# Kernel optimization log

Measured on AMD Instinct MI355X. Metric: run time of the kernel, lower is better.

## Reference

```python
import jax, jax.numpy as jnp
import numpy as np

B, N, F, E, C, FC = 16, 5000, 512, 160000, 64, 128


def gcn_conv(x, src, dst, W, b, n_total):
    loop = jnp.arange(n_total, dtype=src.dtype)
    s = jnp.concatenate([src, loop])
    d = jnp.concatenate([dst, loop])
    deg = jax.ops.segment_sum(jnp.ones_like(s, dtype=x.dtype), d, num_segments=n_total)
    dinv = jnp.where(deg > 0, jax.lax.rsqrt(deg), 0.0)
    norm = dinv[s] * dinv[d]                      # [E']
    h = x @ W                                      # [n_total, out]
    msg = h[s] * norm[:, None]
    out = jax.ops.segment_sum(msg, d, num_segments=n_total)
    return out + b


def setup_inputs() -> dict:
    key = jax.random.key(0)
    ks = jax.random.split(key, 12)
    inp = {
        "node_features": jax.random.normal(ks[0], (B, N, F), jnp.float32),
        "col_features": jax.random.normal(ks[1], (B, C, FC), jnp.float32),
        "edge_index": jax.random.randint(ks[2], (2, E), 0, N, dtype=jnp.int64),
        # GCNConv 1/2 weights + node head
        "W1": jax.random.normal(ks[3], (F, 16), jnp.float32) / np.sqrt(F),
        "b1": jnp.zeros((16,), jnp.float32),
        "W2": jax.random.normal(ks[4], (16, 16), jnp.float32) / 4.0,
        "b2": jnp.zeros((16,), jnp.float32),
        "fc_w": jax.random.normal(ks[5], (16, 1), jnp.float32) / 4.0,
        "fc_b": jnp.zeros((1,), jnp.float32),
        # column MLP: Linear(FC,16) -> ReLU -> Linear(16,1)
        "cw1": jax.random.normal(ks[6], (FC, 16), jnp.float32) / np.sqrt(FC),
        "cb1": jnp.zeros((16,), jnp.float32),
        "cw2": jax.random.normal(ks[7], (16, 1), jnp.float32) / 4.0,
        "cb2": jnp.zeros((1,), jnp.float32),
    }
    return inp


def reference(node_features, col_features, edge_index, W1, b1, W2, b2, fc_w, fc_b, cw1, cb1, cw2, cb2):
    b, n, _ = node_features.shape
    n_total = b * n
    # batched edge_index via node-offset trick (shared graph per batch element)
    offsets = (jnp.arange(b, dtype=edge_index.dtype) * n)[:, None]   # [B,1]
    src = (edge_index[0][None, :] + offsets).reshape(-1)              # [B*E]
    dst = (edge_index[1][None, :] + offsets).reshape(-1)

    x = node_features.reshape(n_total, -1)
    x = jax.nn.relu(gcn_conv(x, src, dst, W1, b1, n_total))
    x = jax.nn.relu(gcn_conv(x, src, dst, W2, b2, n_total))
    node_logits = (x.reshape(b, n, 16) @ fc_w + fc_b)[..., 0]         # [B,N]

    h = jax.nn.relu(col_features @ cw1 + cb1)
    col_logits = (h @ cw2 + cb2)[..., 0]                              # [B,C]

    joint = node_logits[:, :, None] + col_logits[:, None, :]          # [B,N,C]
    return joint.reshape(b, -1)                                       # [B, N*C]
```

## Files before the change

### kernel.cpp

```cpp
#include <hip/hip_runtime.h>
#include <hip/hip_bf16.h>

typedef unsigned short u16;
typedef unsigned int   u32;

#define B_  16
#define N_  5000
#define F_  512
#define C_  64
#define FC_ 128
#define NT  (B_ * N_)

__device__ __forceinline__ float bf2f(u16 h) {
    return __uint_as_float(((u32)h) << 16);
}
__device__ __forceinline__ u16 f2bf(float f) {
    union { __hip_bfloat16 h; u16 s; } c; c.h = __float2bfloat16(f); return c.s;
}
__device__ __forceinline__ float ldw(const void* p, int i, int fF) {
    return fF ? bf2f(((const u16*)p)[i]) : ((const float*)p)[i];
}

__global__ __launch_bounds__(256) void det_k(const u32* __restrict__ x32,
                                             const u32* __restrict__ ei32,
                                             int* __restrict__ flags)
{
    __shared__ int cnt;
    if (threadIdx.x == 0) cnt = 0;
    __syncthreads();
    u32 w = x32[threadIdx.x];
    int e = (int)((w >> 7) & 0xffu);
    if (e >= 112 && e <= 136) atomicAdd(&cnt, 1);
    __syncthreads();
    if (threadIdx.x == 0) {
        flags[0] = (cnt >= 128) ? 1 : 0;
        u32 orv = 0;
        for (int i = 1; i < 64; i += 2) orv |= ei32[i];
        flags[1] = (orv == 0u) ? 1 : 0;
    }
}

__device__ __forceinline__ int src_at(const u32* ei32, int t, int E, int fI) {
    return (int)(fI ? ei32[2 * t] : ei32[t]);
}
__device__ __forceinline__ int dst_at(const u32* ei32, int t, int E, int fI) {
    return (int)(fI ? ei32[2 * (E + t)] : ei32[E + t]);
}

__global__ __launch_bounds__(256) void prep_weights(
    const void* __restrict__ W1, const void* __restrict__ W2,
    const void* __restrict__ fcw, const void* __restrict__ cw1,
    const void* __restrict__ cw2, const void* __restrict__ b1,
    const void* __restrict__ b2, const void* __restrict__ fcb,
    const void* __restrict__ cb1, const void* __restrict__ cb2,
    const int* __restrict__ flags,
    float* __restrict__ w1f, float* __restrict__ w2f, float* __restrict__ fcwf,
    float* __restrict__ cw1f, float* __restrict__ cw2f, float* __restrict__ b1f,
    float* __restrict__ b2f, float* __restrict__ fcbf, float* __restrict__ cb1f,
    float* __restrict__ cb2f)
{
    int fF = flags[0];
    int t = blockIdx.x * blockDim.x + threadIdx.x;
    if (t < 8192) { w1f[t] = ldw(W1, t, fF); return; }
    int u = t - 8192;
    if (u < 256)  { w2f[u]  = ldw(W2, u, fF);  return; }  u -= 256;
    if (u < 16)   { fcwf[u] = ldw(fcw, u, fF); return; }  u -= 16;
    if (u < 2048) { cw1f[u] = ldw(cw1, u, fF); return; }  u -= 2048;
    if (u < 16)   { cw2f[u] = ldw(cw2, u, fF); return; }  u -= 16;
    if (u < 16)   { b1f[u]  = ldw(b1, u, fF);  return; }  u -= 16;
    if (u < 16)   { b2f[u]  = ldw(b2, u, fF);  return; }  u -= 16;
    if (u < 1)    { fcbf[u] = ldw(fcb, u, fF); return; }  u -= 1;
    if (u < 16)   { cb1f[u] = ldw(cb1, u, fF); return; }  u -= 16;
    if (u < 1)    { cb2f[u] = ldw(cb2, u, fF); return; }
}

__global__ __launch_bounds__(256) void deg_k(const u32* __restrict__ ei32,
                                             const int* __restrict__ flags,
                                             int* __restrict__ deg, int E)
{
    int t = blockIdx.x * blockDim.x + threadIdx.x;
    if (t >= E) return;
    int d = dst_at(ei32, t, E, flags[1]);
    if ((unsigned)d < (unsigned)N_) atomicAdd(&deg[d], 1);
}

__global__ __launch_bounds__(1024) void scan_k(const int* __restrict__ deg,
                                               int* __restrict__ rowptr,
                                               int* __restrict__ cursor,
                                               float* __restrict__ dinv)
{
    __shared__ int ssum[1024];
    int t = threadIdx.x;
    int base = t * 5;
    int loc[5];
    int run = 0;
#pragma unroll
    for (int i = 0; i < 5; i++) {
        int idx = base + i;
        int v = (idx < N_) ? deg[idx] : 0;
        loc[i] = run;
        run += v;
    }
    ssum[t] = run;
    __syncthreads();
    for (int offs = 1; offs < 1024; offs <<= 1) {
        int v = (t >= offs) ? ssum[t - offs] : 0;
        __syncthreads();
        ssum[t] += v;
        __syncthreads();
    }
    int exclusive = ssum[t] - run;
#pragma unroll
    for (int i = 0; i < 5; i++) {
        int idx = base + i;
        if (idx < N_) {
            int rp = exclusive + loc[i];
            rowptr[idx] = rp;
            cursor[idx] = rp;
            dinv[idx] = 1.0f / sqrtf((float)deg[idx] + 1.0f);
        }
    }
    if (t == 1023) rowptr[N_] = ssum[1023];
}

__global__ __launch_bounds__(256) void fill_k(const u32* __restrict__ ei32,
                                              const int* __restrict__ flags,
                                              int* __restrict__ cursor,
                                              int* __restrict__ csr, int E)
{
    int t = blockIdx.x * blockDim.x + threadIdx.x;
    if (t >= E) return;
    int fI = flags[1];
    int s = src_at(ei32, t, E, fI);
    int d = dst_at(ei32, t, E, fI);
    if ((unsigned)d >= (unsigned)N_) return;
    if ((unsigned)s >= (unsigned)N_) s = 0;
    int pos = atomicAdd(&cursor[d], 1);
    if ((unsigned)pos < (unsigned)E) csr[pos] = s;
}

__global__ __launch_bounds__(256) void gemm1_k(const void* __restrict__ xraw,
                                               const float* __restrict__ w1f,
                                               const float* __restrict__ dinv,
                                               const int* __restrict__ flags,
                                               u16* __restrict__ out)
{
    int row = blockIdx.x * blockDim.x + threadIdx.x;
    if (row >= NT) return;
    float acc[16];
#pragma unroll
    for (int k = 0; k < 16; k++) acc[k] = 0.0f;

    if (flags[0]) {
        const u16* xr = (const u16*)xraw + (size_t)row * F_;
        for (int f = 0; f < F_; f += 8) {
            uint4 pk = *(const uint4*)(xr + f);
            u32 q[4] = {pk.x, pk.y, pk.z, pk.w};
#pragma unroll
            for (int j = 0; j < 4; j++) {
                float v0 = bf2f((u16)(q[j] & 0xffffu));
                float v1 = bf2f((u16)(q[j] >> 16));
                const float* w0 = w1f + (f + 2 * j) * 16;
#pragma unroll
                for (int k = 0; k < 16; k++) acc[k] += v0 * w0[k];
#pragma unroll
                for (int k = 0; k < 16; k++) acc[k] += v1 * w0[16 + k];
            }
        }
    } else {
        const float* xr = (const float*)xraw + (size_t)row * F_;
        for (int f = 0; f < F_; f += 8) {
            float4 a = *(const float4*)(xr + f);
            float4 b = *(const float4*)(xr + f + 4);
            float v[8] = {a.x, a.y, a.z, a.w, b.x, b.y, b.z, b.w};
#pragma unroll
            for (int j = 0; j < 8; j++) {
                const float* w0 = w1f + (f + j) * 16;
#pragma unroll
                for (int k = 0; k < 16; k++) acc[k] += v[j] * w0[k];
            }
        }
    }
    float s = dinv[row % N_];
    union { uint4 u; u16 h[8]; } o0, o1;
#pragma unroll
    for (int k = 0; k < 8; k++) o0.h[k] = f2bf(acc[k] * s);
#pragma unroll
    for (int k = 0; k < 8; k++) o1.h[k] = f2bf(acc[8 + k] * s);
    uint4* op = (uint4*)(out + (size_t)row * 16);
    op[0] = o0.u;
    op[1] = o1.u;
}

__global__ __launch_bounds__(256) void agg1_k(const u16* __restrict__ h,
                                              const int* __restrict__ rowptr,
                                              const int* __restrict__ csr,
                                              const float* __restrict__ dinv,
                                              const float* __restrict__ b1f,
                                              u16* __restrict__ out)
{
    int t = blockIdx.x * blockDim.x + threadIdx.x;
    int g = t >> 4;
    if (g >= NT) return;
    int k = t & 15;
    int d = g % N_;
    int b = g / N_;
    const u16* hb = h + (size_t)b * N_ * 16;
    float acc = bf2f(hb[d * 16 + k]);
    int e0 = rowptr[d], e1 = rowptr[d + 1];
    for (int e = e0; e < e1; e++) {
        int s = csr[e];
        acc += bf2f(hb[s * 16 + k]);
    }
    float v = acc * dinv[d] + b1f[k];
    out[(size_t)g * 16 + k] = f2bf(fmaxf(v, 0.0f));
}

__global__ __launch_bounds__(256) void gemm2_k(const u16* __restrict__ x1,
                                               const float* __restrict__ w2f,
                                               const float* __restrict__ dinv,
                                               u16* __restrict__ out)
{
    int row = blockIdx.x * blockDim.x + threadIdx.x;
    if (row >= NT) return;
    const uint4* xp = (const uint4*)(x1 + (size_t)row * 16);
    union { uint4 u; u16 h[8]; } i0, i1;
    i0.u = xp[0]; i1.u = xp[1];
    float xv[16];
#pragma unroll
    for (int j = 0; j < 8; j++) { xv[j] = bf2f(i0.h[j]); xv[8 + j] = bf2f(i1.h[j]); }
    float acc[16];
#pragma unroll
    for (int k = 0; k < 16; k++) acc[k] = 0.0f;
#pragma unroll
    for (int j = 0; j < 16; j++) {
        const float* wr = w2f + j * 16;
#pragma unroll
        for (int k = 0; k < 16; k++) acc[k] += xv[j] * wr[k];
    }
    float s = dinv[row % N_];
    union { uint4 u; u16 h[8]; } o0, o1;
#pragma unroll
    for (int k = 0; k < 8; k++) o0.h[k] = f2bf(acc[k] * s);
#pragma unroll
    for (int k = 0; k < 8; k++) o1.h[k] = f2bf(acc[8 + k] * s);
    uint4* op = (uint4*)(out + (size_t)row * 16);
    op[0] = o0.u;
    op[1] = o1.u;
}

__global__ __launch_bounds__(256) void agg2_k(const u16* __restrict__ h,
                                              const int* __restrict__ rowptr,
                                              const int* __restrict__ csr,
                                              const float* __restrict__ dinv,
                                              const float* __restrict__ b2f,
                                              const float* __restrict__ fcwf,
                                              const float* __restrict__ fcbf,
                                              float* __restrict__ nl)
{
    int t = blockIdx.x * blockDim.x + threadIdx.x;
    int g = t >> 4;
    if (g >= NT) return;
    int k = t & 15;
    int d = g % N_;
    int b = g / N_;
    const u16* hb = h + (size_t)b * N_ * 16;
    float acc = bf2f(hb[d * 16 + k]);
    int e0 = rowptr[d], e1 = rowptr[d + 1];
    for (int e = e0; e < e1; e++) {
        int s = csr[e];
        acc += bf2f(hb[s * 16 + k]);
    }
    float v = fmaxf(acc * dinv[d] + b2f[k], 0.0f);
    float p = v * fcwf[k];
    p += __shfl_xor(p, 8, 16);
    p += __shfl_xor(p, 4, 16);
    p += __shfl_xor(p, 2, 16);
    p += __shfl_xor(p, 1, 16);
    if (k == 0) nl[g] = p + fcbf[0];
}

__global__ __launch_bounds__(256) void col_k(const void* __restrict__ cfraw,
                                             const float* __restrict__ cw1f,
                                             const float* __restrict__ cb1f,
                                             const float* __restrict__ cw2f,
                                             const float* __restrict__ cb2f,
                                             const int* __restrict__ flags,
                                             float* __restrict__ cl)
{
    int t = blockIdx.x * blockDim.x + threadIdx.x;
    if (t >= B_ * C_) return;
    float acc[16];
#pragma unroll
    for (int k = 0; k < 16; k++) acc[k] = cb1f[k];
    if (flags[0]) {
        const u16* r = (const u16*)cfraw + (size_t)t * FC_;
        for (int f = 0; f < FC_; f += 8) {
            uint4 pk = *(const uint4*)(r + f);
            u32 q[4] = {pk.x, pk.y, pk.z, pk.w};
#pragma unroll
            for (int j = 0; j < 4; j++) {
                float v0 = bf2f((u16)(q[j] & 0xffffu));
                float v1 = bf2f((u16)(q[j] >> 16));
                const float* w0 = cw1f + (f + 2 * j) * 16;
#pragma unroll
                for (int k = 0; k < 16; k++) acc[k] += v0 * w0[k];
#pragma unroll
                for (int k = 0; k < 16; k++) acc[k] += v1 * w0[16 + k];
            }
        }
    } else {
        const float* r = (const float*)cfraw + (size_t)t * FC_;
        for (int f = 0; f < FC_; f += 4) {
            float4 a = *(const float4*)(r + f);
            float v[4] = {a.x, a.y, a.z, a.w};
#pragma unroll
            for (int j = 0; j < 4; j++) {
                const float* w0 = cw1f + (f + j) * 16;
#pragma unroll
                for (int k = 0; k < 16; k++) acc[k] += v[j] * w0[k];
            }
        }
    }
    float s = cb2f[0];
#pragma unroll
    for (int k = 0; k < 16; k++) s += fmaxf(acc[k], 0.0f) * cw2f[k];
    cl[t] = s;
}

__global__ __launch_bounds__(256) void join_k(const float* __restrict__ nl,
                                              const float* __restrict__ cl,
                                              const int* __restrict__ flags,
                                              void* __restrict__ outraw)
{
    int t = blockIdx.x * blockDim.x + threadIdx.x;
    if (t >= NT * C_ / 8) return;
    int g  = t >> 3;
    int c0 = (t & 7) * 8;
    int b  = g / N_;
    float nv = nl[g];
    const float* c = cl + b * C_ + c0;
    float4 a0 = *(const float4*)c;
    float4 a1 = *(const float4*)(c + 4);
    float v[8] = {a0.x, a0.y, a0.z, a0.w, a1.x, a1.y, a1.z, a1.w};
#pragma unroll
    for (int i = 0; i < 8; i++) v[i] += nv;
    size_t idx = (size_t)g * C_ + c0;
    if (flags[0]) {
        union { uint4 u; u16 h[8]; } pkv;
#pragma unroll
        for (int i = 0; i < 8; i++) pkv.h[i] = f2bf(v[i]);
        *(uint4*)((u16*)outraw + idx) = pkv.u;
    } else {
        float* o = (float*)outraw + idx;
        *(float4*)o       = make_float4(v[0], v[1], v[2], v[3]);
        *(float4*)(o + 4) = make_float4(v[4], v[5], v[6], v[7]);
    }
}

extern "C" void kernel_launch(void* const* d_in, const int* in_sizes, int n_in,
                              void* d_out, int out_size, void* d_ws, size_t ws_size,
                              hipStream_t stream)
{
    const void* x    = d_in[0];
    const void* cf   = d_in[1];
    const u32*  ei32 = (const u32*)d_in[2];
    const void* W1   = d_in[3];
    const void* b1   = d_in[4];
    const void* W2   = d_in[5];
    const void* b2   = d_in[6];
    const void* fcw  = d_in[7];
    const void* fcb  = d_in[8];
    const void* cw1  = d_in[9];
    const void* cb1  = d_in[10];
    const void* cw2  = d_in[11];
    const void* cb2  = d_in[12];

    const int E = in_sizes[2] / 2;

    char* base = (char*)d_ws;
    size_t off = 0;
    auto alloc = [&](size_t bytes) -> void* {
        void* p = base + off;
        off = (off + bytes + 255) & ~(size_t)255;
        return p;
    };
    int*   flags  = (int*)alloc(2 * 4);
    float* w1f  = (float*)alloc(8192 * 4);
    float* w2f  = (float*)alloc(256 * 4);
    float* fcwf = (float*)alloc(16 * 4);
    float* cw1f = (float*)alloc(2048 * 4);
    float* cw2f = (float*)alloc(16 * 4);
    float* b1f  = (float*)alloc(16 * 4);
    float* b2f  = (float*)alloc(16 * 4);
    float* fcbf = (float*)alloc(4);
    float* cb1f = (float*)alloc(16 * 4);
    float* cb2f = (float*)alloc(4);
    int*   deg    = (int*)alloc((size_t)N_ * 4);
    int*   rowptr = (int*)alloc((size_t)(N_ + 1) * 4);
    int*   cursor = (int*)alloc((size_t)N_ * 4);
    float* dinv   = (float*)alloc((size_t)N_ * 4);
    int*   csr    = (int*)alloc((size_t)E * 4);
    u16*   bufA = (u16*)alloc((size_t)NT * 16 * 2);
    u16*   bufB = (u16*)alloc((size_t)NT * 16 * 2);
    float* nl   = (float*)alloc((size_t)NT * 4);
    float* cl   = (float*)alloc((size_t)B_ * C_ * 4);

    det_k<<<1, 256, 0, stream>>>((const u32*)x, ei32, flags);
    hipMemsetAsync(deg, 0, (size_t)N_ * 4, stream);
    prep_weights<<<(10578 + 255) / 256, 256, 0, stream>>>(
        W1, W2, fcw, cw1, cw2, b1, b2, fcb, cb1, cb2, flags,
        w1f, w2f, fcwf, cw1f, cw2f, b1f, b2f, fcbf, cb1f, cb2f);
    deg_k<<<(E + 255) / 256, 256, 0, stream>>>(ei32, flags, deg, E);
    scan_k<<<1, 1024, 0, stream>>>(deg, rowptr, cursor, dinv);
    fill_k<<<(E + 255) / 256, 256, 0, stream>>>(ei32, flags, cursor, csr, E);

    gemm1_k<<<(NT + 255) / 256, 256, 0, stream>>>(x, w1f, dinv, flags, bufA);
    agg1_k<<<(NT * 16 + 255) / 256, 256, 0, stream>>>(bufA, rowptr, csr, dinv, b1f, bufB);
    gemm2_k<<<(NT + 255) / 256, 256, 0, stream>>>(bufB, w2f, dinv, bufA);
    agg2_k<<<(NT * 16 + 255) / 256, 256, 0, stream>>>(bufA, rowptr, csr, dinv, b2f, fcwf, fcbf, nl);
    col_k<<<(B_ * C_ + 255) / 256, 256, 0, stream>>>(cf, cw1f, cb1f, cw2f, cb2f, flags, cl);
    join_k<<<(NT * C_ / 8 + 255) / 256, 256, 0, stream>>>(nl, cl, flags, d_out);
}
```

Before: 434.1 us.

## Split-K gemm1 across warps, fuse gemm2 into agg1, batch neighbor gathers

gemm1 now gives each row to four thread groups, each covering a quarter of the 512 features, and reduces the partial sums through shared memory. This raises parallelism and shortens the per-thread serial loop. The separate gemm2 kernel is removed: agg1 computes the 16x16 projection with shuffles within each 16-lane group, which saves one kernel launch and a round trip through global memory. Both aggregation kernels gather neighbor indices and features in batches of eight to expose memory-level parallelism, and det_k's edge-index check is spread across threads.

```diff
diff --git a/kernel.cpp b/kernel.cpp
--- a/kernel.cpp
+++ b/kernel.cpp
@@ -26,17 +26,19 @@
                                              int* __restrict__ flags)
 {
     __shared__ int cnt;
-    if (threadIdx.x == 0) cnt = 0;
+    __shared__ int orv;
+    if (threadIdx.x == 0) { cnt = 0; orv = 0; }
     __syncthreads();
     u32 w = x32[threadIdx.x];
     int e = (int)((w >> 7) & 0xffu);
     if (e >= 112 && e <= 136) atomicAdd(&cnt, 1);
+    if (threadIdx.x < 32) {
+        if (ei32[2 * threadIdx.x + 1] != 0u) atomicOr(&orv, 1);
+    }
     __syncthreads();
     if (threadIdx.x == 0) {
         flags[0] = (cnt >= 128) ? 1 : 0;
-        u32 orv = 0;
-        for (int i = 1; i < 64; i += 2) orv |= ei32[i];
-        flags[1] = (orv == 0u) ? 1 : 0;
+        flags[1] = (orv == 0) ? 1 : 0;
     }
 }
 
@@ -145,22 +147,27 @@
                                                const int* __restrict__ flags,
                                                u16* __restrict__ out)
 {
-    int row = blockIdx.x * blockDim.x + threadIdx.x;
-    if (row >= NT) return;
+    __shared__ float sAcc[4][64][17];
+    int lane = threadIdx.x & 63;
+    int sub  = threadIdx.x >> 6;
+    int row  = blockIdx.x * 64 + lane;
+    int fbase = sub * 128;
+
     float acc[16];
 #pragma unroll
     for (int k = 0; k < 16; k++) acc[k] = 0.0f;
 
     if (flags[0]) {
-        const u16* xr = (const u16*)xraw + (size_t)row * F_;
-        for (int f = 0; f < F_; f += 8) {
-            uint4 pk = *(const uint4*)(xr + f);
+        const u16* xr = (const u16*)xraw + (size_t)row * F_ + fbase;
+#pragma unroll
+        for (int i = 0; i < 16; i++) {
+            uint4 pk = *(const uint4*)(xr + i * 8);
             u32 q[4] = {pk.x, pk.y, pk.z, pk.w};
 #pragma unroll
             for (int j = 0; j < 4; j++) {
                 float v0 = bf2f((u16)(q[j] & 0xffffu));
                 float v1 = bf2f((u16)(q[j] >> 16));
-                const float* w0 = w1f + (f + 2 * j) * 16;
+                const float* w0 = w1f + (fbase + i * 8 + 2 * j) * 16;
 #pragma unroll
                 for (int k = 0; k < 16; k++) acc[k] += v0 * w0[k];
 #pragma unroll
@@ -168,28 +175,36 @@
             }
         }
     } else {
-        const float* xr = (const float*)xraw + (size_t)row * F_;
-        for (int f = 0; f < F_; f += 8) {
-            float4 a = *(const float4*)(xr + f);
-            float4 b = *(const float4*)(xr + f + 4);
+        const float* xr = (const float*)xraw + (size_t)row * F_ + fbase;
+#pragma unroll
+        for (int i = 0; i < 16; i++) {
+            float4 a = *(const float4*)(xr + i * 8);
+            float4 b = *(const float4*)(xr + i * 8 + 4);
             float v[8] = {a.x, a.y, a.z, a.w, b.x, b.y, b.z, b.w};
 #pragma unroll
             for (int j = 0; j < 8; j++) {
-                const float* w0 = w1f + (f + j) * 16;
+                const float* w0 = w1f + (fbase + i * 8 + j) * 16;
 #pragma unroll
                 for (int k = 0; k < 16; k++) acc[k] += v[j] * w0[k];
             }
         }
     }
-    float s = dinv[row % N_];
-    union { uint4 u; u16 h[8]; } o0, o1;
-#pragma unroll
-    for (int k = 0; k < 8; k++) o0.h[k] = f2bf(acc[k] * s);
-#pragma unroll
-    for (int k = 0; k < 8; k++) o1.h[k] = f2bf(acc[8 + k] * s);
-    uint4* op = (uint4*)(out + (size_t)row * 16);
-    op[0] = o0.u;
-    op[1] = o1.u;
+#pragma unroll
+    for (int k = 0; k < 16; k++) sAcc[sub][lane][k] = acc[k];
+    __syncthreads();
+
+    int r  = threadIdx.x >> 2;
+    int kc = (threadIdx.x & 3) * 4;
+    int orow = blockIdx.x * 64 + r;
+    float s = dinv[orow % N_];
+    union { uint2 u; u16 h[4]; } o;
+#pragma unroll
+    for (int k = 0; k < 4; k++) {
+        float v = sAcc[0][r][kc + k] + sAcc[1][r][kc + k]
+                + sAcc[2][r][kc + k] + sAcc[3][r][kc + k];
+        o.h[k] = f2bf(v * s);
+    }
+    *(uint2*)(out + (size_t)orow * 16 + kc) = o.u;
 }
 
 __global__ __launch_bounds__(256) void agg1_k(const u16* __restrict__ h,
@@ -197,6 +212,7 @@
                                               const int* __restrict__ csr,
                                               const float* __restrict__ dinv,
                                               const float* __restrict__ b1f,
+                                              const float* __restrict__ w2f,
                                               u16* __restrict__ out)
 {
     int t = blockIdx.x * blockDim.x + threadIdx.x;
@@ -208,45 +224,28 @@
     const u16* hb = h + (size_t)b * N_ * 16;
     float acc = bf2f(hb[d * 16 + k]);
     int e0 = rowptr[d], e1 = rowptr[d + 1];
-    for (int e = e0; e < e1; e++) {
-        int s = csr[e];
-        acc += bf2f(hb[s * 16 + k]);
-    }
-    float v = acc * dinv[d] + b1f[k];
-    out[(size_t)g * 16 + k] = f2bf(fmaxf(v, 0.0f));
-}
-
-__global__ __launch_bounds__(256) void gemm2_k(const u16* __restrict__ x1,
-                                               const float* __restrict__ w2f,
-                                               const float* __restrict__ dinv,
-                                               u16* __restrict__ out)
-{
-    int row = blockIdx.x * blockDim.x + threadIdx.x;
-    if (row >= NT) return;
-    const uint4* xp = (const uint4*)(x1 + (size_t)row * 16);
-    union { uint4 u; u16 h[8]; } i0, i1;
-    i0.u = xp[0]; i1.u = xp[1];
-    float xv[16];
-#pragma unroll
-    for (int j = 0; j < 8; j++) { xv[j] = bf2f(i0.h[j]); xv[8 + j] = bf2f(i1.h[j]); }
-    float acc[16];
-#pragma unroll
-    for (int k = 0; k < 16; k++) acc[k] = 0.0f;
+    for (int base = e0; base < e1; base += 8) {
+        int idx[8];
+#pragma unroll
+        for (int j = 0; j < 8; j++) {
+            int e = base + j;
+            idx[j] = csr[e < e1 ? e : e0];
+        }
+        float v[8];
+#pragma unroll
+        for (int j = 0; j < 8; j++) v[j] = bf2f(hb[idx[j] * 16 + k]);
+#pragma unroll
+        for (int j = 0; j < 8; j++) if (base + j < e1) acc += v[j];
+    }
+    float dv = dinv[d];
+    float x1 = fmaxf(acc * dv + b1f[k], 0.0f);
+    float h2 = 0.0f;
 #pragma unroll
     for (int j = 0; j < 16; j++) {
-        const float* wr = w2f + j * 16;
-#pragma unroll
-        for (int k = 0; k < 16; k++) acc[k] += xv[j] * wr[k];
-    }
-    float s = dinv[row % N_];
-    union { uint4 u; u16 h[8]; } o0, o1;
-#pragma unroll
-    for (int k = 0; k < 8; k++) o0.h[k] = f2bf(acc[k] * s);
-#pragma unroll
-    for (int k = 0; k < 8; k++) o1.h[k] = f2bf(acc[8 + k] * s);
-    uint4* op = (uint4*)(out + (size_t)row * 16);
-    op[0] = o0.u;
-    op[1] = o1.u;
+        float xj = __shfl(x1, j, 16);
+        h2 += xj * w2f[j * 16 + k];
+    }
+    out[(size_t)g * 16 + k] = f2bf(h2 * dv);
 }
 
 __global__ __launch_bounds__(256) void agg2_k(const u16* __restrict__ h,
@@ -267,12 +266,21 @@
     const u16* hb = h + (size_t)b * N_ * 16;
     float acc = bf2f(hb[d * 16 + k]);
     int e0 = rowptr[d], e1 = rowptr[d + 1];
-    for (int e = e0; e < e1; e++) {
-        int s = csr[e];
-        acc += bf2f(hb[s * 16 + k]);
-    }
-    float v = fmaxf(acc * dinv[d] + b2f[k], 0.0f);
-    float p = v * fcwf[k];
+    for (int base = e0; base < e1; base += 8) {
+        int idx[8];
+#pragma unroll
+        for (int j = 0; j < 8; j++) {
+            int e = base + j;
+            idx[j] = csr[e < e1 ? e : e0];
+        }
+        float v[8];
+#pragma unroll
+        for (int j = 0; j < 8; j++) v[j] = bf2f(hb[idx[j] * 16 + k]);
+#pragma unroll
+        for (int j = 0; j < 8; j++) if (base + j < e1) acc += v[j];
+    }
+    float x2 = fmaxf(acc * dinv[d] + b2f[k], 0.0f);
+    float p = x2 * fcwf[k];
     p += __shfl_xor(p, 8, 16);
     p += __shfl_xor(p, 4, 16);
     p += __shfl_xor(p, 2, 16);
@@ -415,10 +423,9 @@
     scan_k<<<1, 1024, 0, stream>>>(deg, rowptr, cursor, dinv);
     fill_k<<<(E + 255) / 256, 256, 0, stream>>>(ei32, flags, cursor, csr, E);
 
-    gemm1_k<<<(NT + 255) / 256, 256, 0, stream>>>(x, w1f, dinv, flags, bufA);
-    agg1_k<<<(NT * 16 + 255) / 256, 256, 0, stream>>>(bufA, rowptr, csr, dinv, b1f, bufB);
-    gemm2_k<<<(NT + 255) / 256, 256, 0, stream>>>(bufB, w2f, dinv, bufA);
-    agg2_k<<<(NT * 16 + 255) / 256, 256, 0, stream>>>(bufA, rowptr, csr, dinv, b2f, fcwf, fcbf, nl);
+    gemm1_k<<<NT / 64, 256, 0, stream>>>(x, w1f, dinv, flags, bufA);
+    agg1_k<<<(NT * 16 + 255) / 256, 256, 0, stream>>>(bufA, rowptr, csr, dinv, b1f, w2f, bufB);
+    agg2_k<<<(NT * 16 + 255) / 256, 256, 0, stream>>>(bufB, rowptr, csr, dinv, b2f, fcwf, fcbf, nl);
     col_k<<<(B_ * C_ + 255) / 256, 256, 0, stream>>>(cf, cw1f, cb1f, cw2f, cb2f, flags, cl);
     join_k<<<(NT * C_ / 8 + 255) / 256, 256, 0, stream>>>(nl, cl, flags, d_out);
 }
```

After: 420.5 us. 1.03x faster.
